# Kernel optimization log

Measured on AMD Instinct MI355X. Metric: run time of the kernel, lower is better.

The kernel has to match this reference:

```python
import jax, jax.numpy as jnp
import numpy as np


def _deconcat(values, offsets):
    """Ragged [N, D] + offsets [B+1] -> padded [B, L, D] and valid mask [B, L]."""
    offsets = np.asarray(offsets)
    lengths = np.diff(offsets)
    L = int(lengths.max())
    pos = np.arange(L)
    idx = np.minimum(offsets[:-1, None] + pos[None, :], values.shape[0] - 1)
    valid = pos[None, :] < lengths[:, None]  # [B, L]
    batched = jnp.take(values, jnp.asarray(idx), axis=0)
    batched = batched * jnp.asarray(valid, values.dtype)[:, :, None]
    return batched, jnp.asarray(valid)


def setup_inputs() -> dict:
    B, H, Wd, F, Q, D = 4, 128, 128, 16384, 300, 256
    key = jax.random.key(0)
    ks = jax.random.split(key, 8)
    queries = jax.random.normal(ks[0], (B * Q, D), jnp.float32)
    feature_values = jax.random.normal(ks[1], (B * F, D), jnp.float32)
    hw = jax.random.randint(ks[2], (B * F, 2), 0, H)
    bcol = jnp.repeat(jnp.arange(B), F)[:, None]
    feature_indices = jnp.concatenate([bcol, hw], axis=1).astype(jnp.int32)
    params = {}
    wkeys = jax.random.split(ks[3], 4)
    for i in range(4):
        params[f"W{i}"] = (jax.random.normal(wkeys[i], (D, D), jnp.float32) * 0.02)
        params[f"b{i}"] = jnp.zeros((D,), jnp.float32)
    return dict(
        queries=queries,
        feature_values=feature_values,
        feature_indices=feature_indices,
        query_batch_offsets=jnp.arange(B + 1, dtype=jnp.int32) * Q,
        feature_batch_offsets=jnp.arange(B + 1, dtype=jnp.int32) * F,
        height=H,
        width=Wd,
        **params,
    )


def reference(queries, feature_values, feature_indices,
              query_batch_offsets, feature_batch_offsets,
              height, width, W0, b0, W1, b1, W2, b2, W3, b3):
    q = queries
    for Wl, bl in ((W0, b0), (W1, b1), (W2, b2)):
        q = jax.nn.relu(q @ Wl.T + bl)
    q = q @ W3.T + b3

    bq, qvalid = _deconcat(q, query_batch_offsets)            # [B, Qm, D], [B, Qm]
    bf, fvalid = _deconcat(feature_values, feature_batch_offsets)  # [B, Fm, D]

    # bmm: per-image feature-vs-query logits
    logits = jnp.einsum('bfd,bqd->bfq', bf, bq)               # [B, Fm, Qm]

    # gather each real feature's logit row (undo padding), mask pad queries
    foff = jnp.asarray(np.asarray(feature_batch_offsets))
    b_of_n = feature_indices[:, 0]                            # [N]
    f_of_n = jnp.arange(feature_indices.shape[0]) - foff[b_of_n]
    flat = logits[b_of_n, f_of_n]                             # [N, Qm]
    flat = flat * qvalid.astype(logits.dtype)[b_of_n]

    # dense equivalent of the coalesced sparse COO output (B, H, W, Q);
    # duplicate (b,h,w) indices sum, matching coalesce()
    B, Qm = qvalid.shape
    out = jnp.zeros((B, height, width, Qm), logits.dtype)
    out = out.at[b_of_n, feature_indices[:, 1], feature_indices[:, 2]].add(flat)
    return out
```

## Files before the change

### kernel.cpp

```cpp
#include <hip/hip_runtime.h>
#include <hip/hip_bf16.h>
#include <stdint.h>

typedef __attribute__((ext_vector_type(8))) short bf16x8;
typedef __attribute__((ext_vector_type(4))) float f32x4;

__device__ __forceinline__ unsigned short f2bf(float f) {
    union { float f; unsigned u; } v; v.f = f;
    unsigned u = v.u;
    u += 0x7fff + ((u >> 16) & 1);
    return (unsigned short)(u >> 16);
}

__global__ __launch_bounds__(256) void prep(
    const int* __restrict__ FI, const int* __restrict__ wptr,
    int* __restrict__ cnt, int* __restrict__ slots,
    const float* __restrict__ W0, const float* __restrict__ W1,
    const float* __restrict__ W2, const float* __restrict__ W3,
    unsigned short* __restrict__ wsW,
    int NF, int HW, int wsz, int nbBin)
{
    int blk = blockIdx.x;
    if (blk < nbBin) {
        int i = blk * 256 + threadIdx.x;
        if (i >= NF) return;
        int Wd = *wptr;
        int b = FI[(size_t)i * 3];
        int h = FI[(size_t)i * 3 + 1];
        int w = FI[(size_t)i * 3 + 2];
        int gc = b * HW + h * Wd + w;
        int slot = atomicAdd(&cnt[gc], 1);
        if (slot < 16) slots[(size_t)gc * 16 + slot] = i;
    } else {
        int idx = ((blk - nbBin) * 256 + threadIdx.x) * 4;
        if (idx >= 4 * wsz) return;
        int l = idx / wsz, off = idx - l * wsz;
        const float* Ws = (l == 0) ? W0 : (l == 1) ? W1 : (l == 2) ? W2 : W3;
        float4 v = *(const float4*)(Ws + off);
        ushort4 o; o.x = f2bf(v.x); o.y = f2bf(v.y); o.z = f2bf(v.z); o.w = f2bf(v.w);
        *(ushort4*)(wsW + (size_t)l * wsz + off) = o;
    }
}

__global__ __launch_bounds__(256) void gather_mlp(
    const float* __restrict__ Qf, const unsigned short* __restrict__ Wb,
    const float* __restrict__ b0p, const float* __restrict__ b1p,
    const float* __restrict__ b2p, const float* __restrict__ b3p,
    unsigned short* __restrict__ outQB, int M, int wsz,
    const float* __restrict__ FV, const int* __restrict__ cnt,
    const int* __restrict__ slots, unsigned short* __restrict__ Abuf, int NC,
    int nbM, int nbG)
{
    __shared__ unsigned short At[16 * 264];
    const int tid = threadIdx.x;
    const int wid = tid >> 6, lane = tid & 63, quad = lane >> 4, l16 = lane & 15;

    if (blockIdx.x >= nbM) {
        const int hl  = lane & 31;
        const int hid = lane >> 5;
        const int wg = (blockIdx.x - nbM) * 4 + wid;
        const int nw = nbG * 4;
        for (int cb = wg * 4; cb < NC; cb += nw * 4) {
            int sl = slots[(size_t)cb * 16 + lane];
            #pragma unroll
            for (int i = 0; i < 2; ++i) {
                int j = i * 2 + hid;
                int c = cb + j;
                int nA = cnt[cb + i * 2];     if (nA > 16) nA = 16;
                int nB = cnt[cb + i * 2 + 1]; if (nB > 16) nB = 16;
                int n    = hid ? nB : nA;
                int nmax = nA > nB ? nA : nB;
                float4 a0 = make_float4(0.f, 0.f, 0.f, 0.f);
                float4 a1 = a0;
                for (int s = 0; s < nmax; ++s) {
                    int f = __shfl(sl, j * 16 + s);
                    if (s < n) {
                        const float* src = FV + (size_t)f * 256 + hl * 4;
                        float4 v0 = *(const float4*)(src);
                        float4 v1 = *(const float4*)(src + 128);
                        a0.x += v0.x; a0.y += v0.y; a0.z += v0.z; a0.w += v0.w;
                        a1.x += v1.x; a1.y += v1.y; a1.z += v1.z; a1.w += v1.w;
                    }
                }
                ushort4 o0, o1;
                o0.x = f2bf(a0.x); o0.y = f2bf(a0.y); o0.z = f2bf(a0.z); o0.w = f2bf(a0.w);
                o1.x = f2bf(a1.x); o1.y = f2bf(a1.y); o1.z = f2bf(a1.z); o1.w = f2bf(a1.w);
                unsigned short* dst = Abuf + (size_t)c * 256;
                *(ushort4*)(dst + hl * 4)       = o0;
                *(ushort4*)(dst + 128 + hl * 4) = o1;
            }
        }
        return;
    }

    const int m0 = blockIdx.x * 16;
    #pragma unroll
    for (int i = 0; i < 4; ++i) {
        int c = tid + i * 256;
        int row = c >> 6, kq = (c & 63) * 4;
        int gr = m0 + row; if (gr >= M) gr = M - 1;
        float4 v = *(const float4*)(Qf + (size_t)gr * 256 + kq);
        ushort4 o; o.x = f2bf(v.x); o.y = f2bf(v.y); o.z = f2bf(v.z); o.w = f2bf(v.w);
        *(ushort4*)&At[row * 264 + kq] = o;
    }
    __syncthreads();

    for (int l = 0; l < 4; ++l) {
        const unsigned short* Wl = Wb + (size_t)l * wsz;
        const float* bl = (l == 0) ? b0p : (l == 1) ? b1p : (l == 2) ? b2p : b3p;
        f32x4 acc[4] = {};
        #pragma unroll
        for (int k = 0; k < 256; k += 32) {
            bf16x8 af = *(const bf16x8*)&At[l16 * 264 + k + quad * 8];
            #pragma unroll
            for (int t = 0; t < 4; ++t) {
                int n = wid * 64 + t * 16 + l16;
                bf16x8 bfr = *(const bf16x8*)(Wl + (size_t)n * 256 + k + quad * 8);
                acc[t] = __builtin_amdgcn_mfma_f32_16x16x32_bf16(af, bfr, acc[t], 0, 0, 0);
            }
        }
        __syncthreads();
        #pragma unroll
        for (int t = 0; t < 4; ++t) {
            int n = wid * 64 + t * 16 + l16;
            float bv = bl[n];
            #pragma unroll
            for (int r = 0; r < 4; ++r) {
                int m = quad * 4 + r;
                float v = acc[t][r] + bv;
                if (l < 3) {
                    At[m * 264 + n] = f2bf(fmaxf(v, 0.f));
                } else {
                    if (m0 + m < M) outQB[(size_t)(m0 + m) * 256 + n] = f2bf(v);
                }
            }
        }
        if (l < 3) __syncthreads();
    }
}

__global__ __launch_bounds__(256, 2) void cell_gemm7(
    const unsigned short* __restrict__ Abuf,
    const unsigned short* __restrict__ QB, const int* __restrict__ qoff,
    float* __restrict__ out, int cpb, int HW, int Qstride)
{
    __shared__ unsigned short Bsm[304 * 40];

    const int tid = threadIdx.x;
    const int b   = blockIdx.x / cpb;
    const int c0  = (blockIdx.x - b * cpb) * 128;
    const size_t gc0 = (size_t)b * HW + c0;
    const int q0 = qoff[b];
    int qlen = qoff[b + 1] - q0; if (qlen < 1) qlen = 1;

    const int wid = tid >> 6, lane = tid & 63, quad = lane >> 4, l16 = lane & 15;

    const unsigned short* aptr0 = Abuf + (gc0 + wid * 16 + l16) * 256 + quad * 8;
    const unsigned short* aptr1 = aptr0 + 64 * 256;
    bf16x8 afA0 = *(const bf16x8*)aptr0;
    bf16x8 afA1 = *(const bf16x8*)aptr1;
    f32x4 acc0[19] = {};
    f32x4 acc1[19] = {};

    for (int k0 = 0; k0 < 256; k0 += 32) {
        for (int c = tid; c < 1216; c += 256) {
            int row = c >> 2, kc = (c & 3) * 8;
            int qr = row < qlen ? row : qlen - 1;
            uint4 v = *(const uint4*)(QB + (size_t)(q0 + qr) * 256 + k0 + kc);
            *(uint4*)&Bsm[row * 40 + kc] = v;
        }
        int k1 = (k0 + 32) & 255;
        bf16x8 afB0 = *(const bf16x8*)(aptr0 + k1);
        bf16x8 afB1 = *(const bf16x8*)(aptr1 + k1);
        __syncthreads();
        #pragma unroll
        for (int t = 0; t < 19; ++t) {
            bf16x8 bfr = *(const bf16x8*)&Bsm[(t * 16 + l16) * 40 + quad * 8];
            acc0[t] = __builtin_amdgcn_mfma_f32_16x16x32_bf16(afA0, bfr, acc0[t], 0, 0, 0);
            acc1[t] = __builtin_amdgcn_mfma_f32_16x16x32_bf16(afA1, bfr, acc1[t], 0, 0, 0);
        }
        __syncthreads();
        afA0 = afB0; afA1 = afB1;
    }

    #pragma unroll
    for (int r = 0; r < 4; ++r) {
        int m = quad * 4 + r;
        float* dst0 = out + (gc0 + wid * 16 + m) * Qstride;
        float* dst1 = out + (gc0 + 64 + wid * 16 + m) * Qstride;
        #pragma unroll
        for (int t = 0; t < 19; ++t) {
            int nq = t * 16 + l16;
            if (nq < Qstride) {
                dst0[nq] = (nq < qlen) ? acc0[t][r] : 0.f;
                dst1[nq] = (nq < qlen) ? acc1[t][r] : 0.f;
            }
        }
    }
}

extern "C" void kernel_launch(void* const* d_in, const int* in_sizes, int n_in,
                              void* d_out, int out_size, void* d_ws, size_t ws_size,
                              hipStream_t stream) {
    const float* queries = (const float*)d_in[0];
    const float* FV      = (const float*)d_in[1];
    const int*   FI      = (const int*)d_in[2];
    const int*   qoff    = (const int*)d_in[3];
    const int*   wptr    = (const int*)d_in[6];
    const float* W0 = (const float*)d_in[7];
    const float* b0 = (const float*)d_in[8];
    const float* W1 = (const float*)d_in[9];
    const float* b1 = (const float*)d_in[10];
    const float* W2 = (const float*)d_in[11];
    const float* b2 = (const float*)d_in[12];
    const float* W3 = (const float*)d_in[13];
    const float* b3 = (const float*)d_in[14];
    float* out = (float*)d_out;

    const int NQe = in_sizes[0];
    const int NQ  = NQe / 256;
    const int NF  = in_sizes[1] / 256;
    const int WSZ = in_sizes[7];
    const int B   = in_sizes[3] - 1;
    const int Q   = NQ / B;
    const int HW  = out_size / (B * Q);
    const int NC  = B * HW;
    const int cpb = HW / 128;

    int* cnt   = (int*)d_ws;
    int* slots = cnt + (size_t)NC;
    unsigned short* wsW  = (unsigned short*)(slots + (size_t)NC * 16);
    unsigned short* wsQB = wsW + (size_t)4 * WSZ;
    unsigned short* Abuf = wsQB + (size_t)NQe;

    hipMemsetAsync(cnt, 0, (size_t)NC * sizeof(int), stream);

    const int nbBin = (NF + 255) / 256;
    const int nbW   = (4 * WSZ / 4 + 255) / 256;
    prep<<<nbBin + nbW, 256, 0, stream>>>(FI, wptr, cnt, slots,
                                          W0, W1, W2, W3, wsW, NF, HW, WSZ, nbBin);

    const int nbM = (NQ + 15) / 16;
    const int nbG = 4096;
    gather_mlp<<<nbM + nbG, 256, 0, stream>>>(
        queries, wsW, b0, b1, b2, b3, wsQB, NQ, WSZ,
        FV, cnt, slots, Abuf, NC, nbM, nbG);

    cell_gemm7<<<B * cpb, 256, 0, stream>>>(Abuf, wsQB, qoff, out, cpb, HW, Q);
}
```

Baseline: 200.5 us.

## Double-buffer query tile via direct global-to-LDS loads with XOR swizzle

Replaces the register-staged copy of the query bf16 tile into shared memory with asynchronous global_load_lds DMA into a double-buffered LDS tile. The next k-slice is prefetched while MFMAs run on the current one, which removes one barrier per iteration. An XOR swizzle on the 16-byte chunk index replaces row padding to avoid bank conflicts. LDS use grows to two 320x32 buffers. Correctness depends on the async LDS loads being complete at the single remaining barrier.

```diff
diff --git a/kernel.cpp b/kernel.cpp
--- a/kernel.cpp
+++ b/kernel.cpp
@@ -139,12 +139,12 @@
     }
 }
 
-__global__ __launch_bounds__(256, 2) void cell_gemm7(
+__global__ __launch_bounds__(256, 2) void cell_gemm8(
     const unsigned short* __restrict__ Abuf,
     const unsigned short* __restrict__ QB, const int* __restrict__ qoff,
     float* __restrict__ out, int cpb, int HW, int Qstride)
 {
-    __shared__ unsigned short Bsm[304 * 40];
+    __shared__ unsigned short Bsm[2][320 * 32];
 
     const int tid = threadIdx.x;
     const int b   = blockIdx.x / cpb;
@@ -155,6 +155,25 @@
 
     const int wid = tid >> 6, lane = tid & 63, quad = lane >> 4, l16 = lane & 15;
 
+    const unsigned short* gsrc[5];
+    #pragma unroll
+    for (int i = 0; i < 5; ++i) {
+        int c = tid + i * 256;
+        int row = c >> 2, sub = c & 3;
+        int qr = row < qlen ? row : qlen - 1;
+        gsrc[i] = QB + (size_t)(q0 + qr) * 256 + (sub ^ (row & 3)) * 8;
+    }
+
+    #define STAGE(s, kk)                                                      \
+        { _Pragma("unroll")                                                   \
+          for (int i = 0; i < 5; ++i)                                         \
+              __builtin_amdgcn_global_load_lds(                               \
+                  (const __attribute__((address_space(1))) unsigned int*)     \
+                      (gsrc[i] + (kk)),                                       \
+                  (__attribute__((address_space(3))) unsigned int*)           \
+                      &Bsm[s][(tid + i * 256) * 8],                           \
+                  16, 0, 0); }
+
     const unsigned short* aptr0 = Abuf + (gc0 + wid * 16 + l16) * 256 + quad * 8;
     const unsigned short* aptr1 = aptr0 + 64 * 256;
     bf16x8 afA0 = *(const bf16x8*)aptr0;
@@ -162,26 +181,27 @@
     f32x4 acc0[19] = {};
     f32x4 acc1[19] = {};
 
+    const int rslot = (quad ^ (l16 & 3)) * 8;
+
+    STAGE(0, 0);
+    __syncthreads();
+
     for (int k0 = 0; k0 < 256; k0 += 32) {
-        for (int c = tid; c < 1216; c += 256) {
-            int row = c >> 2, kc = (c & 3) * 8;
-            int qr = row < qlen ? row : qlen - 1;
-            uint4 v = *(const uint4*)(QB + (size_t)(q0 + qr) * 256 + k0 + kc);
-            *(uint4*)&Bsm[row * 40 + kc] = v;
-        }
+        const int cur = (k0 >> 5) & 1;
+        if (k0 + 32 < 256) STAGE(cur ^ 1, k0 + 32);
         int k1 = (k0 + 32) & 255;
         bf16x8 afB0 = *(const bf16x8*)(aptr0 + k1);
         bf16x8 afB1 = *(const bf16x8*)(aptr1 + k1);
-        __syncthreads();
         #pragma unroll
         for (int t = 0; t < 19; ++t) {
-            bf16x8 bfr = *(const bf16x8*)&Bsm[(t * 16 + l16) * 40 + quad * 8];
+            bf16x8 bfr = *(const bf16x8*)&Bsm[cur][(t * 16 + l16) * 32 + rslot];
             acc0[t] = __builtin_amdgcn_mfma_f32_16x16x32_bf16(afA0, bfr, acc0[t], 0, 0, 0);
             acc1[t] = __builtin_amdgcn_mfma_f32_16x16x32_bf16(afA1, bfr, acc1[t], 0, 0, 0);
         }
         __syncthreads();
         afA0 = afB0; afA1 = afB1;
     }
+    #undef STAGE
 
     #pragma unroll
     for (int r = 0; r < 4; ++r) {
@@ -246,5 +266,5 @@
         queries, wsW, b0, b1, b2, b3, wsQB, NQ, WSZ,
         FV, cnt, slots, Abuf, NC, nbM, nbG);
 
-    cell_gemm7<<<B * cpb, 256, 0, stream>>>(Abuf, wsQB, qoff, out, cpb, HW, Q);
-}
+    cell_gemm8<<<B * cpb, 256, 0, stream>>>(Abuf, wsQB, qoff, out, cpb, HW, Q);
+}
```

Result: faster. 192.1 us (-4.2%).
